# Kernel optimization log

Measured on AMD Instinct MI355X. Metric: run time of the kernel, lower is better.

## Reference

```python
import jax, jax.numpy as jnp
import numpy as np
import math

B, S, D, H, G = 2, 2048, 2048, 16, 4
DH = D // H          # 128 head dim
BASE = 1_000_000.0   # RoPE base


def _rope(x):
    # x: (..., S, DH); interleaved RoPE matching the torch module
    pos = jnp.arange(S, dtype=jnp.float32)[:, None]            # (S,1)
    i = jnp.arange(DH // 2, dtype=jnp.float32)                 # (DH/2,)
    omega = jnp.exp(-2.0 * i / DH * math.log(BASE))            # (DH/2,)
    ang = pos * omega                                          # (S, DH/2)
    sin = jnp.repeat(jnp.sin(ang), 2, axis=-1)                 # (S, DH)
    cos = jnp.repeat(jnp.cos(ang), 2, axis=-1)                 # (S, DH)
    xe, xo = x[..., 0::2], x[..., 1::2]
    rot = jnp.stack([-xo, xe], axis=-1).reshape(x.shape)       # (-x1,x0,-x3,x2,...)
    return x * cos + rot * sin


def setup_inputs() -> dict:
    key = jax.random.key(0)
    ks = jax.random.split(key, 5)
    x = jax.random.normal(ks[0], (B, S, D), jnp.float32)
    wq = jax.random.normal(ks[1], (D, D), jnp.float32) * 0.02
    wk = jax.random.normal(ks[2], (DH * G, D), jnp.float32) * 0.02
    wv = jax.random.normal(ks[3], (DH * G, D), jnp.float32) * 0.02
    wo = jax.random.normal(ks[4], (D, D), jnp.float32) * 0.02
    bq = jnp.zeros((D,), jnp.float32)
    bk = jnp.zeros((DH * G,), jnp.float32)
    bv = jnp.zeros((DH * G,), jnp.float32)
    bo = jnp.zeros((D,), jnp.float32)
    masked = jnp.broadcast_to(jnp.triu(jnp.ones((S, S), bool), 1), (B * H, S, S))
    return {"x": x, "wq": wq, "bq": bq, "wk": wk, "bk": bk, "wv": wv,
            "bv": bv, "wo": wo, "bo": bo, "masked": masked}


def reference(x, wq, bq, wk, bk, wv, bv, wo, bo, masked):
    r = H // G  # q heads per kv head; repeat_interleave order -> q head h uses kv h//r
    q = (x @ wq.T + bq).reshape(B, S, H, DH).transpose(0, 2, 1, 3)   # (B,H,S,DH)
    k = (x @ wk.T + bk).reshape(B, S, G, DH).transpose(0, 2, 1, 3)   # (B,G,S,DH)
    v = (x @ wv.T + bv).reshape(B, S, G, DH).transpose(0, 2, 1, 3)   # (B,G,S,DH)
    q = _rope(q)
    k = _rope(k)
    qg = q.reshape(B, G, r, S, DH)                                    # group q heads by kv head
    scores = jnp.einsum('bgrsd,bgtd->bgrst', qg, k)                   # (B,G,r,S,S)
    m = masked.reshape(B, G, r, S, S)
    scores = jnp.where(m, -jnp.inf, scores)
    attn = jax.nn.softmax(scores / math.sqrt(DH), axis=-1)
    out = jnp.einsum('bgrst,bgtd->bgrsd', attn, v)                    # (B,G,r,S,DH)
    out = out.reshape(B, H, S, DH).transpose(0, 2, 1, 3).reshape(B, S, D)
    return out @ wo.T + bo
```

## Files before the change

kernel.cpp:

```cpp
#include <hip/hip_runtime.h>

typedef unsigned short u16;
typedef __attribute__((ext_vector_type(4))) float f32x4;
typedef __attribute__((ext_vector_type(8))) __bf16 bf16x8;
typedef __attribute__((ext_vector_type(8))) unsigned short u16x8;

static __device__ __forceinline__ u16 f2bf(float f) {
  unsigned u = __float_as_uint(f);
  u += 0x7FFFu + ((u >> 16) & 1u);
  return (u16)(u >> 16);
}
static __device__ __forceinline__ float bf2f(u16 h) {
  return __uint_as_float(((unsigned)h) << 16);
}

#define GLOAD16(gsrc, ldst)                                                    \
  __builtin_amdgcn_global_load_lds(                                            \
      (const __attribute__((address_space(1))) unsigned int*)(gsrc),           \
      (__attribute__((address_space(3))) unsigned int*)(ldst), 16, 0, 0)

__global__ void k_cvt_bf16(const float* __restrict__ in, u16* __restrict__ out, int n4) {
  int i = blockIdx.x * blockDim.x + threadIdx.x;
  if (i >= n4) return;
  float4 v = ((const float4*)in)[i];
  ushort4 o;
  o.x = f2bf(v.x); o.y = f2bf(v.y); o.z = f2bf(v.z); o.w = f2bf(v.w);
  ((ushort4*)out)[i] = o;
}

template <int OUT_F32>
__global__ __launch_bounds__(256) void k_gemm_bt(const u16* __restrict__ A,
                                                 const u16* __restrict__ Bt,
                                                 const float* __restrict__ bias,
                                                 void* __restrict__ Cv,
                                                 int M, int N, int K) {
  __shared__ __align__(128) char smem[16384];
  const int tid = threadIdx.x;
  const int lane = tid & 63;
  const int wave = tid >> 6;
  const int m0 = blockIdx.y << 7;
  const int n0 = blockIdx.x << 7;
  const int wr = (wave >> 1) << 6;
  const int wc = (wave & 1) << 6;

  f32x4 acc[4][4];
#pragma unroll
  for (int m = 0; m < 4; ++m)
#pragma unroll
    for (int n = 0; n < 4; ++n) acc[m][n] = (f32x4){0.f, 0.f, 0.f, 0.f};

  const int nk = K >> 5;
  for (int kt = 0; kt < nk; ++kt) {
    const int kk0 = kt << 5;
#pragma unroll
    for (int iss = 0; iss < 4; ++iss) {
      int o = tid * 16 + iss * 4096;
      int lo = o & 8191;
      int row = lo >> 6;
      int cs = ((lo >> 4) & 3) ^ (row & 3);
      const u16* src =
          (o >= 8192 ? Bt + (size_t)(n0 + row) * K : A + (size_t)(m0 + row) * K) + kk0 + cs * 8;
      GLOAD16(src, smem + iss * 4096 + wave * 1024);
    }
    __syncthreads();
    bf16x8 af[4], bfr[4];
#pragma unroll
    for (int m = 0; m < 4; ++m) {
      int r = wr + m * 16 + (lane & 15);
      af[m] = *(const bf16x8*)(smem + r * 64 + (((lane >> 4) ^ (r & 3)) << 4));
    }
#pragma unroll
    for (int n = 0; n < 4; ++n) {
      int r = wc + n * 16 + (lane & 15);
      bfr[n] = *(const bf16x8*)(smem + 8192 + r * 64 + (((lane >> 4) ^ (r & 3)) << 4));
    }
#pragma unroll
    for (int m = 0; m < 4; ++m)
#pragma unroll
      for (int n = 0; n < 4; ++n)
        acc[m][n] = __builtin_amdgcn_mfma_f32_16x16x32_bf16(af[m], bfr[n], acc[m][n], 0, 0, 0);
    __syncthreads();
  }

#pragma unroll
  for (int n = 0; n < 4; ++n) {
    int col = n0 + wc + n * 16 + (lane & 15);
    float bsv = bias[col];
#pragma unroll
    for (int m = 0; m < 4; ++m) {
      int rb = m0 + wr + m * 16 + ((lane >> 4) << 2);
#pragma unroll
      for (int j = 0; j < 4; ++j) {
        float v = acc[m][n][j] + bsv;
        if (OUT_F32)
          ((float*)Cv)[(size_t)(rb + j) * N + col] = v;
        else
          ((u16*)Cv)[(size_t)(rb + j) * N + col] = f2bf(v);
      }
    }
  }
}

__global__ void k_rope(u16* __restrict__ qkv) {
  int t = blockIdx.x * blockDim.x + threadIdx.x;
  int row = t / 1280;
  int p = t - row * 1280;
  int head = p >> 6;
  int i = p & 63;
  int s = row & 2047;
  int col = head < 16 ? (head << 7) + (i << 1) : 2048 + ((head - 16) << 7) + (i << 1);
  u16* ptr = qkv + (size_t)row * 3072 + col;
  ushort2 xv = *(ushort2*)ptr;
  float xe = bf2f(xv.x), xo = bf2f(xv.y);
  float omega = __expf(-0.21586735f * (float)i);
  float ang = (float)s * omega;
  float sn, cs;
  sincosf(ang, &sn, &cs);
  float re = xe * cs - xo * sn;
  float ro = xo * cs + xe * sn;
  if (head < 16) { re *= 0.08838834764831845f; ro *= 0.08838834764831845f; }
  ushort2 ov;
  ov.x = f2bf(re); ov.y = f2bf(ro);
  *(ushort2*)ptr = ov;
}

__global__ __launch_bounds__(256) void k_attn(const u16* __restrict__ qkv,
                                              u16* __restrict__ Ob) {
  __shared__ __align__(128) char smem[43008];
  const int tid = threadIdx.x, lane = tid & 63, wave = tid >> 6;
  const int g16 = lane >> 4;
  const int l15 = lane & 15;
  const int bh = blockIdx.x;
  const int Q0 = (31 - blockIdx.y) << 6;
  const int b = bh >> 4, h = bh & 15, gq = h >> 2;
  const int brow = b << 11;
  const int qcol = h << 7;
  const int kcol = 2048 + (gq << 7);
  const int vcol = 2560 + (gq << 7);

  bf16x8 qf[4];
  {
    int qrow = brow + Q0 + wave * 16 + l15;
    const u16* qp = qkv + (size_t)qrow * 3072 + qcol + (g16 << 3);
#pragma unroll
    for (int kk = 0; kk < 4; ++kk) qf[kk] = *(const bf16x8*)(qp + kk * 32);
  }

  f32x4 oacc[8];
#pragma unroll
  for (int d = 0; d < 8; ++d) oacc[d] = (f32x4){0.f, 0.f, 0.f, 0.f};
  float mrow[4], lrow[4];
#pragma unroll
  for (int j = 0; j < 4; ++j) { mrow[j] = -1e30f; lrow[j] = 0.f; }

  const int nkt = (Q0 >> 6) + 1;
  char* const pbase = smem + 34816 + wave * 2048;

  for (int kt = 0; kt < nkt; ++kt) {
    const size_t krowg = (size_t)(brow + (kt << 6));
#pragma unroll
    for (int iss = 0; iss < 4; ++iss) {
      int o = iss * 4096 + tid * 16;
      int row = o >> 8;
      int cs = ((o >> 4) & 15) ^ (row & 7);
      const u16* src = qkv + (krowg + row) * 3072 + kcol + cs * 8;
      GLOAD16(src, smem + iss * 4096 + wave * 1024);
    }
    {
      const u16* vbase = qkv + krowg * 3072 + vcol;
      const int kp = tid & 31;
#pragma unroll
      for (int u = 0; u < 2; ++u) {
        int d0 = (((tid >> 5) & 7) + u * 8) << 3;
        const u16* s0 = vbase + (size_t)(kp * 2) * 3072 + d0;
        u16x8 r0 = *(const u16x8*)s0;
        u16x8 r1 = *(const u16x8*)(s0 + 3072);
        char* wb = smem + 16384 + kp * 4;
#pragma unroll
        for (int j = 0; j < 8; ++j) {
          unsigned val = (unsigned)r0[j] | ((unsigned)r1[j] << 16);
          *(unsigned*)(wb + (d0 + j) * 144) = val;
        }
      }
    }
    __syncthreads();

    f32x4 sfr[4];
#pragma unroll
    for (int kc = 0; kc < 4; ++kc) {
      f32x4 s = (f32x4){0.f, 0.f, 0.f, 0.f};
      int r = kc * 16 + l15;
#pragma unroll
      for (int kk = 0; kk < 4; ++kk) {
        int byte = r * 256 + ((((kk << 2) + g16) ^ (r & 7)) << 4);
        bf16x8 kf = *(const bf16x8*)(smem + byte);
        s = __builtin_amdgcn_mfma_f32_16x16x32_bf16(qf[kk], kf, s, 0, 0, 0);
      }
      sfr[kc] = s;
    }
    const int qbase = Q0 + wave * 16 + (g16 << 2);
#pragma unroll
    for (int kc = 0; kc < 4; ++kc) {
      int kidx = (kt << 6) + kc * 16 + l15;
#pragma unroll
      for (int j = 0; j < 4; ++j)
        if (kidx > qbase + j) sfr[kc][j] = -3.0e38f;
    }
    float pr[4][4];
#pragma unroll
    for (int j = 0; j < 4; ++j) {
      float mx = fmaxf(fmaxf(sfr[0][j], sfr[1][j]), fmaxf(sfr[2][j], sfr[3][j]));
#pragma unroll
      for (int msk = 8; msk >= 1; msk >>= 1) mx = fmaxf(mx, __shfl_xor(mx, msk));
      float mnew = fmaxf(mrow[j], mx);
      float alpha = __expf(mrow[j] - mnew);
      float rs = 0.f;
#pragma unroll
      for (int kc = 0; kc < 4; ++kc) {
        pr[kc][j] = __expf(sfr[kc][j] - mnew);
        rs += pr[kc][j];
      }
#pragma unroll
      for (int msk = 8; msk >= 1; msk >>= 1) rs += __shfl_xor(rs, msk);
      lrow[j] = lrow[j] * alpha + rs;
      mrow[j] = mnew;
#pragma unroll
      for (int d = 0; d < 8; ++d) oacc[d][j] *= alpha;
    }
#pragma unroll
    for (int kc = 0; kc < 4; ++kc)
#pragma unroll
      for (int j = 0; j < 4; ++j) {
        int q = (g16 << 2) + j;
        int k = kc * 16 + l15;
        int by = q * 128 + (((k >> 3) ^ (q & 7)) << 4) + ((k & 7) << 1);
        *(u16*)(pbase + by) = f2bf(pr[kc][j]);
      }
    asm volatile("s_waitcnt lgkmcnt(0)" ::: "memory");
    __builtin_amdgcn_sched_barrier(0);
#pragma unroll
    for (int ks = 0; ks < 2; ++ks) {
      bf16x8 pf = *(const bf16x8*)(pbase + l15 * 128 +
                                   ((((ks << 2) + g16) ^ (l15 & 7)) << 4));
#pragma unroll
      for (int dt = 0; dt < 8; ++dt) {
        int d = (dt << 4) + l15;
        bf16x8 vf = *(const bf16x8*)(smem + 16384 + d * 144 + (ks << 6) + (g16 << 4));
        oacc[dt] = __builtin_amdgcn_mfma_f32_16x16x32_bf16(pf, vf, oacc[dt], 0, 0, 0);
      }
    }
    __syncthreads();
  }

#pragma unroll
  for (int j = 0; j < 4; ++j) {
    int q = Q0 + wave * 16 + (g16 << 2) + j;
    float inv = 1.0f / lrow[j];
    u16* op = Ob + (size_t)(brow + q) * 2048 + qcol + l15;
#pragma unroll
    for (int dt = 0; dt < 8; ++dt) op[dt * 16] = f2bf(oacc[dt][j] * inv);
  }
}

extern "C" void kernel_launch(void* const* d_in, const int* in_sizes, int n_in,
                              void* d_out, int out_size, void* d_ws, size_t ws_size,
                              hipStream_t stream) {
  const float* x  = (const float*)d_in[0];
  const float* wq = (const float*)d_in[1];
  const float* bq = (const float*)d_in[2];
  const float* wk = (const float*)d_in[3];
  const float* bk = (const float*)d_in[4];
  const float* wv = (const float*)d_in[5];
  const float* bv = (const float*)d_in[6];
  const float* wo = (const float*)d_in[7];
  const float* bo = (const float*)d_in[8];
  float* out = (float*)d_out;

  u16* wsu = (u16*)d_ws;
  u16* xb      = wsu;
  u16* wqkvb   = xb + (size_t)4096 * 2048;
  u16* wob     = wqkvb + (size_t)3072 * 2048;
  u16* qkv     = wob + (size_t)2048 * 2048;
  float* biascat = (float*)(qkv + (size_t)4096 * 3072);
  u16* Ob = xb;

  int n4;
  n4 = (4096 * 2048) / 4;
  k_cvt_bf16<<<(n4 + 255) / 256, 256, 0, stream>>>(x, xb, n4);
  n4 = (2048 * 2048) / 4;
  k_cvt_bf16<<<(n4 + 255) / 256, 256, 0, stream>>>(wq, wqkvb, n4);
  n4 = (512 * 2048) / 4;
  k_cvt_bf16<<<(n4 + 255) / 256, 256, 0, stream>>>(wk, wqkvb + (size_t)2048 * 2048, n4);
  k_cvt_bf16<<<(n4 + 255) / 256, 256, 0, stream>>>(wv, wqkvb + (size_t)2560 * 2048, n4);
  n4 = (2048 * 2048) / 4;
  k_cvt_bf16<<<(n4 + 255) / 256, 256, 0, stream>>>(wo, wob, n4);

  hipMemcpyAsync(biascat, bq, 2048 * sizeof(float), hipMemcpyDeviceToDevice, stream);
  hipMemcpyAsync(biascat + 2048, bk, 512 * sizeof(float), hipMemcpyDeviceToDevice, stream);
  hipMemcpyAsync(biascat + 2560, bv, 512 * sizeof(float), hipMemcpyDeviceToDevice, stream);

  k_gemm_bt<0><<<dim3(3072 / 128, 4096 / 128), 256, 0, stream>>>(
      xb, wqkvb, biascat, qkv, 4096, 3072, 2048);

  k_rope<<<(4096 * 1280) / 256, 256, 0, stream>>>(qkv);

  k_attn<<<dim3(32, 32), 256, 0, stream>>>(qkv, Ob);

  k_gemm_bt<1><<<dim3(2048 / 128, 4096 / 128), 256, 0, stream>>>(
      Ob, wob, bo, out, 4096, 2048, 2048);
}
```

Measured before the change: 276.8 us.

## Write transposed V from QKV GEMM and process 128 queries per attention block

The QKV GEMM epilogue now writes V already transposed into a separate buffer, so the attention kernel can async-load V^T tiles straight into LDS instead of transposing V in registers on every tile. The attention block now covers 128 queries (32 per wave), so each K/V tile loaded into LDS is reused for two query sub-tiles, halving K/V traffic per query. The five fp32-to-bf16 conversion launches are merged into one kernel. The costs are more registers per wave under a three-blocks occupancy hint, and some waves idle on the diagonal tiles.

```diff
diff --git a/kernel.cpp b/kernel.cpp
--- a/kernel.cpp
+++ b/kernel.cpp
@@ -19,20 +19,30 @@
       (const __attribute__((address_space(1))) unsigned int*)(gsrc),           \
       (__attribute__((address_space(3))) unsigned int*)(ldst), 16, 0, 0)
 
-__global__ void k_cvt_bf16(const float* __restrict__ in, u16* __restrict__ out, int n4) {
+__global__ void k_cvt5(const float* __restrict__ x, const float* __restrict__ wq,
+                       const float* __restrict__ wk, const float* __restrict__ wv,
+                       const float* __restrict__ wo, u16* __restrict__ xb,
+                       u16* __restrict__ wqkvb, u16* __restrict__ wob) {
   int i = blockIdx.x * blockDim.x + threadIdx.x;
-  if (i >= n4) return;
-  float4 v = ((const float4*)in)[i];
+  const float* src;
+  u16* dst;
+  if (i < 2097152) { src = x + (size_t)i * 4; dst = xb + (size_t)i * 4; }
+  else if (i < 3145728) { src = wq + (size_t)(i - 2097152) * 4; dst = wqkvb + (size_t)(i - 2097152) * 4; }
+  else if (i < 3407872) { src = wk + (size_t)(i - 3145728) * 4; dst = wqkvb + (size_t)(i - 2097152) * 4; }
+  else if (i < 3670016) { src = wv + (size_t)(i - 3407872) * 4; dst = wqkvb + (size_t)(i - 2097152) * 4; }
+  else { src = wo + (size_t)(i - 3670016) * 4; dst = wob + (size_t)(i - 3670016) * 4; }
+  float4 v = *(const float4*)src;
   ushort4 o;
   o.x = f2bf(v.x); o.y = f2bf(v.y); o.z = f2bf(v.z); o.w = f2bf(v.w);
-  ((ushort4*)out)[i] = o;
-}
-
-template <int OUT_F32>
+  *(ushort4*)dst = o;
+}
+
+template <int MODE>
 __global__ __launch_bounds__(256) void k_gemm_bt(const u16* __restrict__ A,
                                                  const u16* __restrict__ Bt,
                                                  const float* __restrict__ bias,
                                                  void* __restrict__ Cv,
+                                                 u16* __restrict__ VtG,
                                                  int M, int N, int K) {
   __shared__ __align__(128) char smem[16384];
   const int tid = threadIdx.x;
@@ -82,6 +92,28 @@
     __syncthreads();
   }
 
+  if (MODE == 2 && n0 >= 2560) {
+#pragma unroll
+    for (int n = 0; n < 4; ++n) {
+      int col = n0 + wc + n * 16 + (lane & 15);
+      int vd = col - 2560;
+      float bsv = bias[col];
+      u16* vrow = VtG + ((size_t)vd) * 2048;
+#pragma unroll
+      for (int m = 0; m < 4; ++m) {
+        int rb = m0 + wr + m * 16 + ((lane >> 4) << 2);
+        int bb = rb >> 11, ss = rb & 2047;
+        ushort4 w;
+        w.x = f2bf(acc[m][n][0] + bsv);
+        w.y = f2bf(acc[m][n][1] + bsv);
+        w.z = f2bf(acc[m][n][2] + bsv);
+        w.w = f2bf(acc[m][n][3] + bsv);
+        *(ushort4*)(vrow + (size_t)bb * (512 * 2048) + ss) = w;
+      }
+    }
+    return;
+  }
+
 #pragma unroll
   for (int n = 0; n < 4; ++n) {
     int col = n0 + wc + n * 16 + (lane & 15);
@@ -92,7 +124,7 @@
 #pragma unroll
       for (int j = 0; j < 4; ++j) {
         float v = acc[m][n][j] + bsv;
-        if (OUT_F32)
+        if (MODE == 1)
           ((float*)Cv)[(size_t)(rb + j) * N + col] = v;
         else
           ((u16*)Cv)[(size_t)(rb + j) * N + col] = f2bf(v);
@@ -124,37 +156,44 @@
   *(ushort2*)ptr = ov;
 }
 
-__global__ __launch_bounds__(256) void k_attn(const u16* __restrict__ qkv,
-                                              u16* __restrict__ Ob) {
-  __shared__ __align__(128) char smem[43008];
+__global__ __launch_bounds__(256, 3) void k_attn(const u16* __restrict__ qkv,
+                                                 const u16* __restrict__ vtg,
+                                                 u16* __restrict__ Ob) {
+  __shared__ __align__(128) char smem[49152];
   const int tid = threadIdx.x, lane = tid & 63, wave = tid >> 6;
   const int g16 = lane >> 4;
   const int l15 = lane & 15;
   const int bh = blockIdx.x;
-  const int Q0 = (31 - blockIdx.y) << 6;
+  const int Q0 = (15 - blockIdx.y) << 7;
   const int b = bh >> 4, h = bh & 15, gq = h >> 2;
   const int brow = b << 11;
   const int qcol = h << 7;
   const int kcol = 2048 + (gq << 7);
-  const int vcol = 2560 + (gq << 7);
-
-  bf16x8 qf[4];
-  {
-    int qrow = brow + Q0 + wave * 16 + l15;
+  const u16* vt_base = vtg + ((size_t)((b << 2) + gq) << 7) * 2048;
+
+  bf16x8 qf[2][4];
+#pragma unroll
+  for (int qi = 0; qi < 2; ++qi) {
+    int qrow = brow + Q0 + wave * 32 + qi * 16 + l15;
     const u16* qp = qkv + (size_t)qrow * 3072 + qcol + (g16 << 3);
 #pragma unroll
-    for (int kk = 0; kk < 4; ++kk) qf[kk] = *(const bf16x8*)(qp + kk * 32);
-  }
-
-  f32x4 oacc[8];
-#pragma unroll
-  for (int d = 0; d < 8; ++d) oacc[d] = (f32x4){0.f, 0.f, 0.f, 0.f};
-  float mrow[4], lrow[4];
-#pragma unroll
-  for (int j = 0; j < 4; ++j) { mrow[j] = -1e30f; lrow[j] = 0.f; }
-
-  const int nkt = (Q0 >> 6) + 1;
-  char* const pbase = smem + 34816 + wave * 2048;
+    for (int kk = 0; kk < 4; ++kk) qf[qi][kk] = *(const bf16x8*)(qp + kk * 32);
+  }
+
+  f32x4 oacc[2][8];
+#pragma unroll
+  for (int qi = 0; qi < 2; ++qi)
+#pragma unroll
+    for (int d = 0; d < 8; ++d) oacc[qi][d] = (f32x4){0.f, 0.f, 0.f, 0.f};
+  float mrow[2][4], lrow[2][4];
+#pragma unroll
+  for (int qi = 0; qi < 2; ++qi)
+#pragma unroll
+    for (int j = 0; j < 4; ++j) { mrow[qi][j] = -1e30f; lrow[qi][j] = 0.f; }
+
+  const int nkt = (Q0 >> 6) + 2;
+  const int qmaxw = Q0 + wave * 32 + 31;
+  char* const pbase = smem + 32768 + wave * 4096;
 
   for (int kt = 0; kt < nkt; ++kt) {
     const size_t krowg = (size_t)(brow + (kt << 6));
@@ -166,100 +205,100 @@
       const u16* src = qkv + (krowg + row) * 3072 + kcol + cs * 8;
       GLOAD16(src, smem + iss * 4096 + wave * 1024);
     }
-    {
-      const u16* vbase = qkv + krowg * 3072 + vcol;
-      const int kp = tid & 31;
-#pragma unroll
-      for (int u = 0; u < 2; ++u) {
-        int d0 = (((tid >> 5) & 7) + u * 8) << 3;
-        const u16* s0 = vbase + (size_t)(kp * 2) * 3072 + d0;
-        u16x8 r0 = *(const u16x8*)s0;
-        u16x8 r1 = *(const u16x8*)(s0 + 3072);
-        char* wb = smem + 16384 + kp * 4;
-#pragma unroll
-        for (int j = 0; j < 8; ++j) {
-          unsigned val = (unsigned)r0[j] | ((unsigned)r1[j] << 16);
-          *(unsigned*)(wb + (d0 + j) * 144) = val;
+#pragma unroll
+    for (int iss = 0; iss < 4; ++iss) {
+      int o = iss * 4096 + tid * 16;
+      int d = o >> 7;
+      int cs = ((o >> 4) & 7) ^ (d & 7);
+      const u16* src = vt_base + (size_t)d * 2048 + (kt << 6) + cs * 8;
+      GLOAD16(src, smem + 16384 + iss * 4096 + wave * 1024);
+    }
+    __syncthreads();
+
+    if ((kt << 6) <= qmaxw) {
+      f32x4 sfr[2][4];
+#pragma unroll
+      for (int qi = 0; qi < 2; ++qi)
+#pragma unroll
+        for (int kc = 0; kc < 4; ++kc) sfr[qi][kc] = (f32x4){0.f, 0.f, 0.f, 0.f};
+#pragma unroll
+      for (int kc = 0; kc < 4; ++kc) {
+        int r = kc * 16 + l15;
+#pragma unroll
+        for (int kk = 0; kk < 4; ++kk) {
+          int byte = r * 256 + ((((kk << 2) + g16) ^ (r & 7)) << 4);
+          bf16x8 kf = *(const bf16x8*)(smem + byte);
+          sfr[0][kc] = __builtin_amdgcn_mfma_f32_16x16x32_bf16(qf[0][kk], kf, sfr[0][kc], 0, 0, 0);
+          sfr[1][kc] = __builtin_amdgcn_mfma_f32_16x16x32_bf16(qf[1][kk], kf, sfr[1][kc], 0, 0, 0);
         }
       }
+#pragma unroll
+      for (int qi = 0; qi < 2; ++qi) {
+        const int qb = Q0 + wave * 32 + qi * 16 + (g16 << 2);
+#pragma unroll
+        for (int kc = 0; kc < 4; ++kc) {
+          int kidx = (kt << 6) + kc * 16 + l15;
+#pragma unroll
+          for (int j = 0; j < 4; ++j)
+            if (kidx > qb + j) sfr[qi][kc][j] = -3.0e38f;
+        }
+#pragma unroll
+        for (int j = 0; j < 4; ++j) {
+          float mx = fmaxf(fmaxf(sfr[qi][0][j], sfr[qi][1][j]),
+                           fmaxf(sfr[qi][2][j], sfr[qi][3][j]));
+#pragma unroll
+          for (int msk = 8; msk >= 1; msk >>= 1) mx = fmaxf(mx, __shfl_xor(mx, msk));
+          float mnew = fmaxf(mrow[qi][j], mx);
+          float alpha = __expf(mrow[qi][j] - mnew);
+          const int q = qi * 16 + (g16 << 2) + j;
+          const int qkey = (q >> 1) & 7;
+          float rs = 0.f;
+#pragma unroll
+          for (int kc = 0; kc < 4; ++kc) {
+            float p = __expf(sfr[qi][kc][j] - mnew);
+            rs += p;
+            int k = kc * 16 + l15;
+            *(u16*)(pbase + q * 128 + (((k >> 3) ^ qkey) << 4) + ((k & 7) << 1)) = f2bf(p);
+          }
+#pragma unroll
+          for (int msk = 8; msk >= 1; msk >>= 1) rs += __shfl_xor(rs, msk);
+          lrow[qi][j] = lrow[qi][j] * alpha + rs;
+          mrow[qi][j] = mnew;
+#pragma unroll
+          for (int dt = 0; dt < 8; ++dt) oacc[qi][dt][j] *= alpha;
+        }
+      }
+      asm volatile("s_waitcnt lgkmcnt(0)" ::: "memory");
+      __builtin_amdgcn_sched_barrier(0);
+#pragma unroll
+      for (int ks = 0; ks < 2; ++ks) {
+        bf16x8 pf0 = *(const bf16x8*)(pbase + l15 * 128 +
+                                      ((((ks << 2) + g16) ^ (l15 >> 1)) << 4));
+        bf16x8 pf1 = *(const bf16x8*)(pbase + (16 + l15) * 128 +
+                                      ((((ks << 2) + g16) ^ (l15 >> 1)) << 4));
+#pragma unroll
+        for (int dt = 0; dt < 8; ++dt) {
+          int d = (dt << 4) + l15;
+          bf16x8 vf = *(const bf16x8*)(smem + 16384 + d * 128 +
+                                       ((((ks << 2) + g16) ^ (d & 7)) << 4));
+          oacc[0][dt] = __builtin_amdgcn_mfma_f32_16x16x32_bf16(pf0, vf, oacc[0][dt], 0, 0, 0);
+          oacc[1][dt] = __builtin_amdgcn_mfma_f32_16x16x32_bf16(pf1, vf, oacc[1][dt], 0, 0, 0);
+        }
+      }
     }
     __syncthreads();
-
-    f32x4 sfr[4];
-#pragma unroll
-    for (int kc = 0; kc < 4; ++kc) {
-      f32x4 s = (f32x4){0.f, 0.f, 0.f, 0.f};
-      int r = kc * 16 + l15;
-#pragma unroll
-      for (int kk = 0; kk < 4; ++kk) {
-        int byte = r * 256 + ((((kk << 2) + g16) ^ (r & 7)) << 4);
-        bf16x8 kf = *(const bf16x8*)(smem + byte);
-        s = __builtin_amdgcn_mfma_f32_16x16x32_bf16(qf[kk], kf, s, 0, 0, 0);
-      }
-      sfr[kc] = s;
-    }
-    const int qbase = Q0 + wave * 16 + (g16 << 2);
-#pragma unroll
-    for (int kc = 0; kc < 4; ++kc) {
-      int kidx = (kt << 6) + kc * 16 + l15;
-#pragma unroll
-      for (int j = 0; j < 4; ++j)
-        if (kidx > qbase + j) sfr[kc][j] = -3.0e38f;
-    }
-    float pr[4][4];
+  }
+
+#pragma unroll
+  for (int qi = 0; qi < 2; ++qi)
 #pragma unroll
     for (int j = 0; j < 4; ++j) {
-      float mx = fmaxf(fmaxf(sfr[0][j], sfr[1][j]), fmaxf(sfr[2][j], sfr[3][j]));
-#pragma unroll
-      for (int msk = 8; msk >= 1; msk >>= 1) mx = fmaxf(mx, __shfl_xor(mx, msk));
-      float mnew = fmaxf(mrow[j], mx);
-      float alpha = __expf(mrow[j] - mnew);
-      float rs = 0.f;
-#pragma unroll
-      for (int kc = 0; kc < 4; ++kc) {
-        pr[kc][j] = __expf(sfr[kc][j] - mnew);
-        rs += pr[kc][j];
-      }
-#pragma unroll
-      for (int msk = 8; msk >= 1; msk >>= 1) rs += __shfl_xor(rs, msk);
-      lrow[j] = lrow[j] * alpha + rs;
-      mrow[j] = mnew;
-#pragma unroll
-      for (int d = 0; d < 8; ++d) oacc[d][j] *= alpha;
-    }
-#pragma unroll
-    for (int kc = 0; kc < 4; ++kc)
-#pragma unroll
-      for (int j = 0; j < 4; ++j) {
-        int q = (g16 << 2) + j;
-        int k = kc * 16 + l15;
-        int by = q * 128 + (((k >> 3) ^ (q & 7)) << 4) + ((k & 7) << 1);
-        *(u16*)(pbase + by) = f2bf(pr[kc][j]);
-      }
-    asm volatile("s_waitcnt lgkmcnt(0)" ::: "memory");
-    __builtin_amdgcn_sched_barrier(0);
-#pragma unroll
-    for (int ks = 0; ks < 2; ++ks) {
-      bf16x8 pf = *(const bf16x8*)(pbase + l15 * 128 +
-                                   ((((ks << 2) + g16) ^ (l15 & 7)) << 4));
-#pragma unroll
-      for (int dt = 0; dt < 8; ++dt) {
-        int d = (dt << 4) + l15;
-        bf16x8 vf = *(const bf16x8*)(smem + 16384 + d * 144 + (ks << 6) + (g16 << 4));
-        oacc[dt] = __builtin_amdgcn_mfma_f32_16x16x32_bf16(pf, vf, oacc[dt], 0, 0, 0);
-      }
-    }
-    __syncthreads();
-  }
-
-#pragma unroll
-  for (int j = 0; j < 4; ++j) {
-    int q = Q0 + wave * 16 + (g16 << 2) + j;
-    float inv = 1.0f / lrow[j];
-    u16* op = Ob + (size_t)(brow + q) * 2048 + qcol + l15;
-#pragma unroll
-    for (int dt = 0; dt < 8; ++dt) op[dt * 16] = f2bf(oacc[dt][j] * inv);
-  }
+      int q = Q0 + wave * 32 + qi * 16 + (g16 << 2) + j;
+      float inv = 1.0f / lrow[qi][j];
+      u16* op = Ob + (size_t)(brow + q) * 2048 + qcol + l15;
+#pragma unroll
+      for (int dt = 0; dt < 8; ++dt) op[dt * 16] = f2bf(oacc[qi][dt][j] * inv);
+    }
 }
 
 extern "C" void kernel_launch(void* const* d_in, const int* in_sizes, int n_in,
@@ -282,30 +321,22 @@
   u16* wob     = wqkvb + (size_t)3072 * 2048;
   u16* qkv     = wob + (size_t)2048 * 2048;
   float* biascat = (float*)(qkv + (size_t)4096 * 3072);
+  u16* vtg     = (u16*)(biascat + 3072);
   u16* Ob = xb;
 
-  int n4;
-  n4 = (4096 * 2048) / 4;
-  k_cvt_bf16<<<(n4 + 255) / 256, 256, 0, stream>>>(x, xb, n4);
-  n4 = (2048 * 2048) / 4;
-  k_cvt_bf16<<<(n4 + 255) / 256, 256, 0, stream>>>(wq, wqkvb, n4);
-  n4 = (512 * 2048) / 4;
-  k_cvt_bf16<<<(n4 + 255) / 256, 256, 0, stream>>>(wk, wqkvb + (size_t)2048 * 2048, n4);
-  k_cvt_bf16<<<(n4 + 255) / 256, 256, 0, stream>>>(wv, wqkvb + (size_t)2560 * 2048, n4);
-  n4 = (2048 * 2048) / 4;
-  k_cvt_bf16<<<(n4 + 255) / 256, 256, 0, stream>>>(wo, wob, n4);
+  k_cvt5<<<18432, 256, 0, stream>>>(x, wq, wk, wv, wo, xb, wqkvb, wob);
 
   hipMemcpyAsync(biascat, bq, 2048 * sizeof(float), hipMemcpyDeviceToDevice, stream);
   hipMemcpyAsync(biascat + 2048, bk, 512 * sizeof(float), hipMemcpyDeviceToDevice, stream);
   hipMemcpyAsync(biascat + 2560, bv, 512 * sizeof(float), hipMemcpyDeviceToDevice, stream);
 
-  k_gemm_bt<0><<<dim3(3072 / 128, 4096 / 128), 256, 0, stream>>>(
-      xb, wqkvb, biascat, qkv, 4096, 3072, 2048);
+  k_gemm_bt<2><<<dim3(3072 / 128, 4096 / 128), 256, 0, stream>>>(
+      xb, wqkvb, biascat, qkv, vtg, 4096, 3072, 2048);
 
   k_rope<<<(4096 * 1280) / 256, 256, 0, stream>>>(qkv);
 
-  k_attn<<<dim3(32, 32), 256, 0, stream>>>(qkv, Ob);
+  k_attn<<<dim3(32, 16), 256, 0, stream>>>(qkv, vtg, Ob);
 
   k_gemm_bt<1><<<dim3(2048 / 128, 4096 / 128), 256, 0, stream>>>(
-      Ob, wob, bo, out, 4096, 2048, 2048);
-}
+      Ob, wob, bo, out, nullptr, 4096, 2048, 2048);
+}
```

Measured after the change: 389.9 us. +40.8%, slower.
